# Performance work log

Hardware: AMD Instinct MI355X
Metric: run time of the kernel (lower is better)

Reference implementation:

```python
import jax, jax.numpy as jnp
import numpy as np
import math

B, S, D, H = 4, 2048, 1024, 16
HD = D // H
MASKED_BIAS = -10000.0

def setup_inputs() -> dict:
    key = jax.random.key(0)
    k1, k2, k3, k4, k5 = jax.random.split(key, 5)
    scale = 0.02
    return {
        "hidden_states": jax.random.normal(k1, (B, S, D), dtype=jnp.float32),
        "w_attn": jax.random.normal(k2, (D, 3 * D), dtype=jnp.float32) * scale,
        "b_attn": jnp.zeros((3 * D,), dtype=jnp.float32),
        "w_proj": jax.random.normal(k3, (D, D), dtype=jnp.float32) * scale,
        "b_proj": jnp.zeros((D,), dtype=jnp.float32),
    }

def reference(hidden_states, w_attn, b_attn, w_proj, b_proj):
    b, s, d = hidden_states.shape
    qkv = hidden_states @ w_attn + b_attn                      # [B,S,3D]
    q, k, v = jnp.split(qkv, 3, axis=-1)
    # split heads -> [B,H,S,HD]
    def split_heads(x):
        return x.reshape(b, s, H, HD).transpose(0, 2, 1, 3)
    q, k, v = split_heads(q), split_heads(k), split_heads(v)
    scores = jnp.einsum("bhqd,bhkd->bhqk", q, k) / math.sqrt(HD)
    causal = jnp.tril(jnp.ones((s, s), dtype=bool))
    scores = jnp.where(causal[None, None], scores, jnp.float32(MASKED_BIAS))
    probs = jax.nn.softmax(scores, axis=-1)
    ctx = jnp.einsum("bhqk,bhkd->bhqd", probs, v)
    ctx = ctx.transpose(0, 2, 1, 3).reshape(b, s, d)           # merge heads
    return ctx @ w_proj + b_proj
```

## Files before the change

### kernel.cpp

```cpp
#include <hip/hip_runtime.h>

typedef unsigned short u16;
typedef __attribute__((ext_vector_type(8))) short short8;
typedef __attribute__((ext_vector_type(4))) float f32x4;
typedef __attribute__((ext_vector_type(4))) unsigned u32x4;

#define Bq 4
#define Sq 2048
#define Dq 1024
#define Hq 16
#define HDq 64
#define BSq 8192

#define QSCALE 0.18033688011112042f

__device__ __forceinline__ u16 f2bf(float f) {
  unsigned u = __builtin_bit_cast(unsigned, f);
  unsigned r = u + 0x7fffu + ((u >> 16) & 1u);
  return (u16)(r >> 16);
}

__device__ __forceinline__ unsigned pk2(float a, float b) {
  unsigned ua = __builtin_bit_cast(unsigned, a) + 0x8000u;
  unsigned ub = __builtin_bit_cast(unsigned, b) + 0x8000u;
  return __builtin_amdgcn_perm(ub, ua, 0x07060302u);
}

__device__ __forceinline__ unsigned cvtpk(float a, float b) {
  unsigned r;
  asm("v_cvt_pk_bf16_f32 %0, %1, %2" : "=v"(r) : "v"(a), "v"(b));
  return r;
}

__device__ __forceinline__ void gl_lds16(const u16* g, u16* l) {
  __builtin_amdgcn_global_load_lds((const __attribute__((address_space(1))) unsigned int*)g,
                                   (__attribute__((address_space(3))) unsigned int*)l, 16, 0, 0);
}

__device__ __forceinline__ int kperm(int kk) {
  return ((kk & 0x10) << 1) | ((kk & 0x0C) << 1) | ((kk & 0x20) >> 3) | (kk & 3);
}

__global__ void cvt_kernel(const float* __restrict__ in, u16* __restrict__ out, int n8) {
  int i = blockIdx.x * blockDim.x + threadIdx.x;
  if (i >= n8) return;
  float4 v0 = reinterpret_cast<const float4*>(in)[2 * i];
  float4 v1 = reinterpret_cast<const float4*>(in)[2 * i + 1];
  u32x4 o;
  o[0] = pk2(v0.x, v0.y); o[1] = pk2(v0.z, v0.w);
  o[2] = pk2(v1.x, v1.y); o[3] = pk2(v1.z, v1.w);
  reinterpret_cast<u32x4*>(out)[i] = o;
}

__global__ void transpose_cvt(const float* __restrict__ in, u16* __restrict__ out, int R, int C) {
  __shared__ float tile[32][33];
  int c0 = blockIdx.x * 32, r0 = blockIdx.y * 32;
  for (int i = threadIdx.y; i < 32; i += 8)
    tile[i][threadIdx.x] = in[(size_t)(r0 + i) * C + c0 + threadIdx.x];
  __syncthreads();
  for (int i = threadIdx.y; i < 32; i += 8)
    out[(size_t)(c0 + i) * R + r0 + threadIdx.x] = f2bf(tile[threadIdx.x][i]);
}

template<int EPI>
__global__ __launch_bounds__(256)
void gemm_bt(const u16* __restrict__ A, const u16* __restrict__ Bt,
             const float* __restrict__ bias,
             u16* __restrict__ Qb, u16* __restrict__ Kb, u16* __restrict__ Vt,
             float* __restrict__ Out, int Kdim) {
  __shared__ __align__(16) u16 As[128 * 64];
  __shared__ __align__(16) u16 Bs[128 * 64];
  int tid = threadIdx.x;
  int lane = tid & 63;
  int wid = tid >> 6;
  int wr = wid >> 1, wc = wid & 1;
  constexpr int NX = (EPI == 0) ? 24 : 8;
  constexpr int NWG = NX * 64;
  int orig = (int)blockIdx.x + NX * (int)blockIdx.y;
  int swz = (orig & 7) * (NWG >> 3) + (orig >> 3);
  int m0 = (swz / NX) * 128, n0 = (swz % NX) * 128;
  int l15 = lane & 15, g = lane >> 4;
  f32x4 acc[4][4] = {};

  const u16* aP[4];
  const u16* bP[4];
#pragma unroll
  for (int i = 0; i < 4; ++i) {
    int f = i * 256 + tid;
    int row = f >> 3, slot = f & 7;
    int src = ((slot ^ (row & 7)) << 3);
    aP[i] = &A[(size_t)(m0 + row) * Kdim + src];
    bP[i] = &Bt[(size_t)(n0 + row) * Kdim + src];
  }

  int nk = Kdim >> 6;
  for (int t = 0; t < nk; ++t) {
    __syncthreads();
    int ko = t << 6;
#pragma unroll
    for (int i = 0; i < 4; ++i) {
      int f = i * 256 + tid;
      gl_lds16(aP[i] + ko, &As[f << 3]);
      gl_lds16(bP[i] + ko, &Bs[f << 3]);
    }
    __syncthreads();
#pragma unroll
    for (int ksub = 0; ksub < 2; ++ksub) {
      int sl = (((ksub << 2) | g) ^ (l15 & 7)) << 3;
      short8 af[4], bfr[4];
#pragma unroll
      for (int m = 0; m < 4; ++m)
        af[m] = *reinterpret_cast<const short8*>(&As[(wr * 64 + m * 16 + l15) * 64 + sl]);
#pragma unroll
      for (int n = 0; n < 4; ++n)
        bfr[n] = *reinterpret_cast<const short8*>(&Bs[(wc * 64 + n * 16 + l15) * 64 + sl]);
      __builtin_amdgcn_s_setprio(1);
#pragma unroll
      for (int m = 0; m < 4; ++m)
#pragma unroll
        for (int n = 0; n < 4; ++n)
          acc[m][n] = __builtin_amdgcn_mfma_f32_16x16x32_bf16(af[m], bfr[n], acc[m][n], 0, 0, 0);
      __builtin_amdgcn_s_setprio(0);
    }
  }

  int bb = (m0 + wr * 64) >> 11;
  int sb = (m0 + wr * 64) & 2047;

  if (EPI == 1) {
#pragma unroll
    for (int m = 0; m < 4; ++m)
#pragma unroll
      for (int n = 0; n < 4; ++n) {
        int gcol = n0 + wc * 64 + n * 16 + l15;
        float bv = bias[gcol];
#pragma unroll
        for (int r = 0; r < 4; ++r) {
          int grow = m0 + wr * 64 + m * 16 + g * 4 + r;
          Out[(size_t)grow * 1024 + gcol] = acc[m][n][r] + bv;
        }
      }
  } else if (n0 < 1024) {
#pragma unroll
    for (int n = 0; n < 4; ++n) {
      int col = n0 + wc * 64 + n * 16 + l15;
      int hh = col >> 6, d = col & 63;
      float bv = bias[col];
      u16* qb = &Qb[(((size_t)(bb * 16 + hh) * 2048 + sb) << 6) + d];
#pragma unroll
      for (int m = 0; m < 4; ++m)
#pragma unroll
        for (int r = 0; r < 4; ++r)
          qb[(size_t)(m * 16 + g * 4 + r) << 6] = f2bf((acc[m][n][r] + bv) * QSCALE);
    }
  } else if (n0 < 2048) {
#pragma unroll
    for (int n = 0; n < 4; ++n) {
      int col = n0 - 1024 + wc * 64 + n * 16 + l15;
      int hh = col >> 6, d = col & 63;
      float bv = bias[1024 + col];
      u16* kb = &Kb[(((size_t)(bb * 16 + hh) * 2048 + sb) << 6) + d];
#pragma unroll
      for (int m = 0; m < 4; ++m)
#pragma unroll
        for (int r = 0; r < 4; ++r)
          kb[(size_t)(m * 16 + g * 4 + r) << 6] = f2bf(acc[m][n][r] + bv);
    }
  } else {
#pragma unroll
    for (int n = 0; n < 4; ++n) {
      int cc = n0 - 2048 + wc * 64 + n * 16 + l15;
      int hh = cc >> 6, d = cc & 63;
      float bv = bias[2048 + cc];
      u16* dst = &Vt[((size_t)(bb * 16 + hh) * 64 + d) * 2048 + sb];
      u32x4 lo, hi;
      lo[0] = pk2(acc[0][n][0] + bv, acc[0][n][1] + bv);
      lo[1] = pk2(acc[0][n][2] + bv, acc[0][n][3] + bv);
      lo[2] = pk2(acc[2][n][0] + bv, acc[2][n][1] + bv);
      lo[3] = pk2(acc[2][n][2] + bv, acc[2][n][3] + bv);
      hi[0] = pk2(acc[1][n][0] + bv, acc[1][n][1] + bv);
      hi[1] = pk2(acc[1][n][2] + bv, acc[1][n][3] + bv);
      hi[2] = pk2(acc[3][n][0] + bv, acc[3][n][1] + bv);
      hi[3] = pk2(acc[3][n][2] + bv, acc[3][n][3] + bv);
      *reinterpret_cast<u32x4*>(dst + g * 8) = lo;
      *reinterpret_cast<u32x4*>(dst + 32 + g * 8) = hi;
    }
  }
}

__global__ __launch_bounds__(256, 2)
void attn_kernel(const u16* __restrict__ Qb, const u16* __restrict__ Kb,
                 const u16* __restrict__ Vt, u16* __restrict__ Ctx) {
  __shared__ __align__(16) u16 lds[2][2][8][512];
  int tid = threadIdx.x, lane = tid & 63, w = tid >> 6;
  int l15 = lane & 15, g = lane >> 4;
  int bh = blockIdx.y;
  const u16* Qh = Qb + (size_t)bh * Sq * HDq;
  const u16* Kh = Kb + (size_t)bh * Sq * HDq;
  const u16* Vh = Vt + (size_t)bh * HDq * Sq;
  int b = bh >> 4, h = bh & 15;

  int tileA = 31 - (int)blockIdx.x, tileB = (int)blockIdx.x;
  int nkA = tileA + 1;
  int ntot = nkA + tileB + 1;

  const u16* ksrc = Kh + (size_t)(16 * w + l15) * 64 + 8 * g;
  const u16* vsrc = Vh + (size_t)(16 * w + l15) * Sq + 8 * g;
  const u16* kpre = ksrc + 4096;
  const u16* vpre = vsrc + 64;

  int tile = tileA;
  int qbase = tileA * 64 + w * 16;

  short8 qf[2];
  qf[0] = *reinterpret_cast<const short8*>(&Qh[(size_t)(qbase + l15) * 64 + 8 * g]);
  qf[1] = *reinterpret_cast<const short8*>(&Qh[(size_t)(qbase + l15) * 64 + 32 + 8 * g]);

  u16 onebits = (l15 == 0) ? (u16)0x3F80 : (u16)0;
  short8 vones;
#pragma unroll
  for (int i = 0; i < 8; ++i) vones[i] = (short)onebits;

  f32x4 acc[4] = {};
  f32x4 acc_l = {};

  gl_lds16(ksrc,      &lds[0][0][2 * w][0]);
  gl_lds16(ksrc + 32, &lds[0][0][2 * w + 1][0]);
  gl_lds16(vsrc,      &lds[0][1][2 * w][0]);
  gl_lds16(vsrc + 32, &lds[0][1][2 * w + 1][0]);
  __syncthreads();
  int cur = 0;
  int kb = 0;

#pragma unroll 1
  for (int it = 0; it < ntot; ++it) {
    bool lastA = (it == nkA - 1);
    int k0 = kb << 6;

    if (it + 1 < ntot) {
      gl_lds16(kpre,      &lds[cur ^ 1][0][2 * w][0]);
      gl_lds16(kpre + 32, &lds[cur ^ 1][0][2 * w + 1][0]);
      gl_lds16(vpre,      &lds[cur ^ 1][1][2 * w][0]);
      gl_lds16(vpre + 32, &lds[cur ^ 1][1][2 * w + 1][0]);
      if (it == nkA - 2) { kpre = ksrc; vpre = vsrc; }
      else               { kpre += 4096; vpre += 64; }
    }

    short8 kf[4][2], vbf[4][2];
#pragma unroll
    for (int j = 0; j < 4; ++j) {
      kf[j][0] = *reinterpret_cast<const short8*>(&lds[cur][0][2 * j][lane * 8]);
      kf[j][1] = *reinterpret_cast<const short8*>(&lds[cur][0][2 * j + 1][lane * 8]);
    }
#pragma unroll
    for (int n = 0; n < 4; ++n) {
      vbf[n][0] = *reinterpret_cast<const short8*>(&lds[cur][1][2 * n][lane * 8]);
      vbf[n][1] = *reinterpret_cast<const short8*>(&lds[cur][1][2 * n + 1][lane * 8]);
    }

    f32x4 sj[4];
    __builtin_amdgcn_s_setprio(1);
#pragma unroll
    for (int j = 0; j < 4; ++j) {
      f32x4 z = {};
      z = __builtin_amdgcn_mfma_f32_16x16x32_bf16(kf[j][0], qf[0], z, 0, 0, 0);
      z = __builtin_amdgcn_mfma_f32_16x16x32_bf16(kf[j][1], qf[1], z, 0, 0, 0);
      sj[j] = z;
    }
    __builtin_amdgcn_s_setprio(0);

    if (kb == tile) {
      int q = qbase + l15;
#pragma unroll
      for (int j = 0; j < 4; ++j)
#pragma unroll
        for (int r = 0; r < 4; ++r)
          if (k0 + 16 * j + 4 * g + r > q) sj[j][r] = -1e30f;
    }

    float p[4][4];
#pragma unroll
    for (int j = 0; j < 4; ++j)
#pragma unroll
      for (int r = 0; r < 4; ++r)
        p[j][r] = exp2f(sj[j][r]);

    u32x4 w0, w1;
    w0[0] = cvtpk(p[0][0], p[0][1]); w0[1] = cvtpk(p[0][2], p[0][3]);
    w0[2] = cvtpk(p[2][0], p[2][1]); w0[3] = cvtpk(p[2][2], p[2][3]);
    w1[0] = cvtpk(p[1][0], p[1][1]); w1[1] = cvtpk(p[1][2], p[1][3]);
    w1[2] = cvtpk(p[3][0], p[3][1]); w1[3] = cvtpk(p[3][2], p[3][3]);
    short8 pa0 = __builtin_bit_cast(short8, w0);
    short8 pa1 = __builtin_bit_cast(short8, w1);
    __builtin_amdgcn_s_setprio(1);
#pragma unroll
    for (int n = 0; n < 4; ++n) {
      acc[n] = __builtin_amdgcn_mfma_f32_16x16x32_bf16(pa0, vbf[n][0], acc[n], 0, 0, 0);
      acc[n] = __builtin_amdgcn_mfma_f32_16x16x32_bf16(pa1, vbf[n][1], acc[n], 0, 0, 0);
    }
    acc_l = __builtin_amdgcn_mfma_f32_16x16x32_bf16(pa0, vones, acc_l, 0, 0, 0);
    acc_l = __builtin_amdgcn_mfma_f32_16x16x32_bf16(pa1, vones, acc_l, 0, 0, 0);
    __builtin_amdgcn_s_setprio(0);

    kb++;
    if (lastA) {
      float lf[4];
#pragma unroll
      for (int r = 0; r < 4; ++r) lf[r] = __shfl(acc_l[r], 16 * g);
#pragma unroll
      for (int r = 0; r < 4; ++r) {
        float inv = 1.0f / lf[r];
        int row = qbase + 4 * g + r;
        size_t obase = ((size_t)(b * Sq + row)) * Dq + h * 64;
#pragma unroll
        for (int n = 0; n < 4; ++n)
          Ctx[obase + 16 * n + l15] = f2bf(acc[n][r] * inv);
      }
      qbase = tileB * 64 + w * 16;
      tile = tileB;
      kb = 0;
      qf[0] = *reinterpret_cast<const short8*>(&Qh[(size_t)(qbase + l15) * 64 + 8 * g]);
      qf[1] = *reinterpret_cast<const short8*>(&Qh[(size_t)(qbase + l15) * 64 + 32 + 8 * g]);
#pragma unroll
      for (int n = 0; n < 4; ++n) acc[n] = f32x4{};
      acc_l = f32x4{};
    }

    __syncthreads();
    cur ^= 1;
  }

  {
    float lf[4];
#pragma unroll
    for (int r = 0; r < 4; ++r) lf[r] = __shfl(acc_l[r], 16 * g);
#pragma unroll
    for (int r = 0; r < 4; ++r) {
      float inv = 1.0f / lf[r];
      int row = qbase + 4 * g + r;
      size_t obase = ((size_t)(b * Sq + row)) * Dq + h * 64;
#pragma unroll
      for (int n = 0; n < 4; ++n)
        Ctx[obase + 16 * n + l15] = f2bf(acc[n][r] * inv);
    }
  }
}

extern "C" void kernel_launch(void* const* d_in, const int* in_sizes, int n_in,
                              void* d_out, int out_size, void* d_ws, size_t ws_size,
                              hipStream_t stream) {
  const float* X  = (const float*)d_in[0];
  const float* Wa = (const float*)d_in[1];
  const float* Ba = (const float*)d_in[2];
  const float* Wp = (const float*)d_in[3];
  const float* Bp = (const float*)d_in[4];
  float* Out = (float*)d_out;

  u16* ws  = (u16*)d_ws;
  u16* Xb  = ws;
  u16* WaT = Xb  + (size_t)BSq * Dq;
  u16* WpT = WaT + (size_t)3 * Dq * Dq;
  u16* Qb  = WpT + (size_t)Dq * Dq;
  u16* Kb  = Qb  + (size_t)Bq * Hq * Sq * HDq;
  u16* Vt  = Kb  + (size_t)Bq * Hq * Sq * HDq;
  u16* Ctx = Vt  + (size_t)Bq * Hq * Sq * HDq;

  cvt_kernel<<<(BSq * Dq / 8 + 255) / 256, 256, 0, stream>>>(X, Xb, BSq * Dq / 8);
  transpose_cvt<<<dim3(3 * Dq / 32, Dq / 32), dim3(32, 8), 0, stream>>>(Wa, WaT, Dq, 3 * Dq);
  transpose_cvt<<<dim3(Dq / 32, Dq / 32), dim3(32, 8), 0, stream>>>(Wp, WpT, Dq, Dq);
  gemm_bt<0><<<dim3(3 * Dq / 128, BSq / 128), 256, 0, stream>>>(Xb, WaT, Ba, Qb, Kb, Vt, nullptr, Dq);
  attn_kernel<<<dim3(16, Bq * Hq), 256, 0, stream>>>(Qb, Kb, Vt, Ctx);
  gemm_bt<1><<<dim3(Dq / 128, BSq / 128), 256, 0, stream>>>(Ctx, WpT, Bp, nullptr, nullptr, nullptr, Out, Dq);
}
```

Before: 183.2 us.

## Use 128-row query tiles per block instead of paired causal tiles

Each block now processes one 128-row query tile, with each wave handling two 16-row sub-tiles. Each K/V tile loaded into shared memory is reused for twice as many query rows. This replaces the old scheme that paired a late and an early 64-row tile per block to balance causal work. In exchange the blocks become unbalanced (2 to 32 iterations each), the block count depends on the launch grid, and register pressure rises from the doubled accumulators.

```diff
diff --git a/kernel.cpp b/kernel.cpp
--- a/kernel.cpp
+++ b/kernel.cpp
@@ -200,29 +200,29 @@
   const u16* Vh = Vt + (size_t)bh * HDq * Sq;
   int b = bh >> 4, h = bh & 15;
 
-  int tileA = 31 - (int)blockIdx.x, tileB = (int)blockIdx.x;
-  int nkA = tileA + 1;
-  int ntot = nkA + tileB + 1;
+  int qb = 15 - (int)blockIdx.x;
+  int nk = 2 * qb + 2;
+  int qbase = qb * 128 + w * 32;
 
   const u16* ksrc = Kh + (size_t)(16 * w + l15) * 64 + 8 * g;
   const u16* vsrc = Vh + (size_t)(16 * w + l15) * Sq + 8 * g;
   const u16* kpre = ksrc + 4096;
   const u16* vpre = vsrc + 64;
 
-  int tile = tileA;
-  int qbase = tileA * 64 + w * 16;
-
-  short8 qf[2];
-  qf[0] = *reinterpret_cast<const short8*>(&Qh[(size_t)(qbase + l15) * 64 + 8 * g]);
-  qf[1] = *reinterpret_cast<const short8*>(&Qh[(size_t)(qbase + l15) * 64 + 32 + 8 * g]);
+  short8 qf[2][2];
+#pragma unroll
+  for (int s = 0; s < 2; ++s)
+#pragma unroll
+    for (int hh = 0; hh < 2; ++hh)
+      qf[s][hh] = *reinterpret_cast<const short8*>(&Qh[(size_t)(qbase + 16 * s + l15) * 64 + 32 * hh + 8 * g]);
 
   u16 onebits = (l15 == 0) ? (u16)0x3F80 : (u16)0;
   short8 vones;
 #pragma unroll
   for (int i = 0; i < 8; ++i) vones[i] = (short)onebits;
 
-  f32x4 acc[4] = {};
-  f32x4 acc_l = {};
+  f32x4 acc[2][4] = {};
+  f32x4 acc_l[2] = {};
 
   gl_lds16(ksrc,      &lds[0][0][2 * w][0]);
   gl_lds16(ksrc + 32, &lds[0][0][2 * w + 1][0]);
@@ -230,20 +230,17 @@
   gl_lds16(vsrc + 32, &lds[0][1][2 * w + 1][0]);
   __syncthreads();
   int cur = 0;
-  int kb = 0;
 
 #pragma unroll 1
-  for (int it = 0; it < ntot; ++it) {
-    bool lastA = (it == nkA - 1);
+  for (int kb = 0; kb < nk; ++kb) {
     int k0 = kb << 6;
 
-    if (it + 1 < ntot) {
+    if (kb + 1 < nk) {
       gl_lds16(kpre,      &lds[cur ^ 1][0][2 * w][0]);
       gl_lds16(kpre + 32, &lds[cur ^ 1][0][2 * w + 1][0]);
       gl_lds16(vpre,      &lds[cur ^ 1][1][2 * w][0]);
       gl_lds16(vpre + 32, &lds[cur ^ 1][1][2 * w + 1][0]);
-      if (it == nkA - 2) { kpre = ksrc; vpre = vsrc; }
-      else               { kpre += 4096; vpre += 64; }
+      kpre += 4096; vpre += 64;
     }
 
     short8 kf[4][2], vbf[4][2];
@@ -258,90 +255,72 @@
       vbf[n][1] = *reinterpret_cast<const short8*>(&lds[cur][1][2 * n + 1][lane * 8]);
     }
 
-    f32x4 sj[4];
-    __builtin_amdgcn_s_setprio(1);
-#pragma unroll
-    for (int j = 0; j < 4; ++j) {
-      f32x4 z = {};
-      z = __builtin_amdgcn_mfma_f32_16x16x32_bf16(kf[j][0], qf[0], z, 0, 0, 0);
-      z = __builtin_amdgcn_mfma_f32_16x16x32_bf16(kf[j][1], qf[1], z, 0, 0, 0);
-      sj[j] = z;
-    }
-    __builtin_amdgcn_s_setprio(0);
-
-    if (kb == tile) {
-      int q = qbase + l15;
+#pragma unroll
+    for (int s = 0; s < 2; ++s) {
+      int q0s = qbase + 16 * s;
+
+      f32x4 sj[4];
+      __builtin_amdgcn_s_setprio(1);
+#pragma unroll
+      for (int j = 0; j < 4; ++j) {
+        f32x4 z = {};
+        z = __builtin_amdgcn_mfma_f32_16x16x32_bf16(kf[j][0], qf[s][0], z, 0, 0, 0);
+        z = __builtin_amdgcn_mfma_f32_16x16x32_bf16(kf[j][1], qf[s][1], z, 0, 0, 0);
+        sj[j] = z;
+      }
+      __builtin_amdgcn_s_setprio(0);
+
+      if (k0 + 63 > q0s) {
+        int q = q0s + l15;
+#pragma unroll
+        for (int j = 0; j < 4; ++j)
+#pragma unroll
+          for (int r = 0; r < 4; ++r)
+            if (k0 + 16 * j + 4 * g + r > q) sj[j][r] = -1e30f;
+      }
+
+      float p[4][4];
 #pragma unroll
       for (int j = 0; j < 4; ++j)
 #pragma unroll
         for (int r = 0; r < 4; ++r)
-          if (k0 + 16 * j + 4 * g + r > q) sj[j][r] = -1e30f;
-    }
-
-    float p[4][4];
-#pragma unroll
-    for (int j = 0; j < 4; ++j)
-#pragma unroll
-      for (int r = 0; r < 4; ++r)
-        p[j][r] = exp2f(sj[j][r]);
-
-    u32x4 w0, w1;
-    w0[0] = cvtpk(p[0][0], p[0][1]); w0[1] = cvtpk(p[0][2], p[0][3]);
-    w0[2] = cvtpk(p[2][0], p[2][1]); w0[3] = cvtpk(p[2][2], p[2][3]);
-    w1[0] = cvtpk(p[1][0], p[1][1]); w1[1] = cvtpk(p[1][2], p[1][3]);
-    w1[2] = cvtpk(p[3][0], p[3][1]); w1[3] = cvtpk(p[3][2], p[3][3]);
-    short8 pa0 = __builtin_bit_cast(short8, w0);
-    short8 pa1 = __builtin_bit_cast(short8, w1);
-    __builtin_amdgcn_s_setprio(1);
-#pragma unroll
-    for (int n = 0; n < 4; ++n) {
-      acc[n] = __builtin_amdgcn_mfma_f32_16x16x32_bf16(pa0, vbf[n][0], acc[n], 0, 0, 0);
-      acc[n] = __builtin_amdgcn_mfma_f32_16x16x32_bf16(pa1, vbf[n][1], acc[n], 0, 0, 0);
-    }
-    acc_l = __builtin_amdgcn_mfma_f32_16x16x32_bf16(pa0, vones, acc_l, 0, 0, 0);
-    acc_l = __builtin_amdgcn_mfma_f32_16x16x32_bf16(pa1, vones, acc_l, 0, 0, 0);
-    __builtin_amdgcn_s_setprio(0);
-
-    kb++;
-    if (lastA) {
-      float lf[4];
-#pragma unroll
-      for (int r = 0; r < 4; ++r) lf[r] = __shfl(acc_l[r], 16 * g);
-#pragma unroll
-      for (int r = 0; r < 4; ++r) {
-        float inv = 1.0f / lf[r];
-        int row = qbase + 4 * g + r;
-        size_t obase = ((size_t)(b * Sq + row)) * Dq + h * 64;
-#pragma unroll
-        for (int n = 0; n < 4; ++n)
-          Ctx[obase + 16 * n + l15] = f2bf(acc[n][r] * inv);
+          p[j][r] = exp2f(sj[j][r]);
+
+      u32x4 w0, w1;
+      w0[0] = cvtpk(p[0][0], p[0][1]); w0[1] = cvtpk(p[0][2], p[0][3]);
+      w0[2] = cvtpk(p[2][0], p[2][1]); w0[3] = cvtpk(p[2][2], p[2][3]);
+      w1[0] = cvtpk(p[1][0], p[1][1]); w1[1] = cvtpk(p[1][2], p[1][3]);
+      w1[2] = cvtpk(p[3][0], p[3][1]); w1[3] = cvtpk(p[3][2], p[3][3]);
+      short8 pa0 = __builtin_bit_cast(short8, w0);
+      short8 pa1 = __builtin_bit_cast(short8, w1);
+      __builtin_amdgcn_s_setprio(1);
+#pragma unroll
+      for (int n = 0; n < 4; ++n) {
+        acc[s][n] = __builtin_amdgcn_mfma_f32_16x16x32_bf16(pa0, vbf[n][0], acc[s][n], 0, 0, 0);
+        acc[s][n] = __builtin_amdgcn_mfma_f32_16x16x32_bf16(pa1, vbf[n][1], acc[s][n], 0, 0, 0);
       }
-      qbase = tileB * 64 + w * 16;
-      tile = tileB;
-      kb = 0;
-      qf[0] = *reinterpret_cast<const short8*>(&Qh[(size_t)(qbase + l15) * 64 + 8 * g]);
-      qf[1] = *reinterpret_cast<const short8*>(&Qh[(size_t)(qbase + l15) * 64 + 32 + 8 * g]);
-#pragma unroll
-      for (int n = 0; n < 4; ++n) acc[n] = f32x4{};
-      acc_l = f32x4{};
+      acc_l[s] = __builtin_amdgcn_mfma_f32_16x16x32_bf16(pa0, vones, acc_l[s], 0, 0, 0);
+      acc_l[s] = __builtin_amdgcn_mfma_f32_16x16x32_bf16(pa1, vones, acc_l[s], 0, 0, 0);
+      __builtin_amdgcn_s_setprio(0);
     }
 
     __syncthreads();
     cur ^= 1;
   }
 
-  {
+#pragma unroll
+  for (int s = 0; s < 2; ++s) {
     float lf[4];
 #pragma unroll
-    for (int r = 0; r < 4; ++r) lf[r] = __shfl(acc_l[r], 16 * g);
+    for (int r = 0; r < 4; ++r) lf[r] = __shfl(acc_l[s][r], 16 * g);
 #pragma unroll
     for (int r = 0; r < 4; ++r) {
       float inv = 1.0f / lf[r];
-      int row = qbase + 4 * g + r;
+      int row = qbase + 16 * s + 4 * g + r;
       size_t obase = ((size_t)(b * Sq + row)) * Dq + h * 64;
 #pragma unroll
       for (int n = 0; n < 4; ++n)
-        Ctx[obase + 16 * n + l15] = f2bf(acc[n][r] * inv);
+        Ctx[obase + 16 * n + l15] = f2bf(acc[s][n][r] * inv);
     }
   }
 }
```

Result: slower. 206.3 us (+12.6%).
